# Performance work log

Hardware: AMD Instinct MI355X
Metric: run time of the kernel (lower is better)

Reference implementation:

```python
import jax, jax.numpy as jnp
import numpy as np

TEMP = 1.0  # composition softmax temperature

def _bank_topk(x, U, V, logits, top_k):
    # softmax over primitive logits, select top-k, renormalize, fused low-rank projection
    w = jax.nn.softmax(logits / TEMP)                     # [P]
    tw, ti = jax.lax.top_k(w, top_k)                      # [k], [k]
    tw = tw / tw.sum()
    Us = U[ti]                                            # [k, d_in, r]
    Vs = V[ti]                                            # [k, r, d_out]
    h = jnp.einsum('bsd,kdr->bksr', x, Us)                # low-rank bottleneck
    return jnp.einsum('bksr,kro,k->bso', h, Vs, tw)       # weighted fuse

def reference(x, q_U, q_V, k_U, k_V, v_U, v_V, q_logits, k_logits, v_logits, out_w, top_k):
    B, S, _ = x.shape
    H, D = 16, 64
    q = _bank_topk(x, q_U, q_V, q_logits, top_k)
    k = _bank_topk(x, k_U, k_V, k_logits, top_k)
    v = _bank_topk(x, v_U, v_V, v_logits, top_k)
    q = q.reshape(B, S, H, D).transpose(0, 2, 1, 3)       # [B,H,S,D]
    k = k.reshape(B, S, H, D).transpose(0, 2, 1, 3)
    v = v.reshape(B, S, H, D).transpose(0, 2, 1, 3)
    scale = 1.0 / jnp.sqrt(jnp.asarray(D, dtype=x.dtype))
    scores = jnp.einsum('bhqd,bhkd->bhqk', q, k) * scale  # [B,H,S,S]
    causal = jnp.triu(jnp.ones((S, S), dtype=bool), 1)
    scores = jnp.where(causal[None, None], jnp.finfo(x.dtype).min, scores)
    probs = jax.nn.softmax(scores, axis=-1)
    out = jnp.einsum('bhqk,bhkd->bhqd', probs, v)
    out = out.transpose(0, 2, 1, 3).reshape(B, S, H * D)
    return out @ out_w.T                                   # nn.Linear(H*D, d_model, bias=False)

def setup_inputs() -> dict:
    key = jax.random.key(0)
    ks = jax.random.split(key, 11)
    P, d, r = 16, 1024, 64
    B, S = 4, 1024
    f = jnp.float32
    inp = {
        'x': jax.random.normal(ks[0], (B, S, d), f),
        'q_U': jax.random.normal(ks[1], (P, d, r), f) * (1.0 / np.sqrt(d)),
        'q_V': jax.random.normal(ks[2], (P, r, d), f) * (1.0 / np.sqrt(r)),
        'k_U': jax.random.normal(ks[3], (P, d, r), f) * (1.0 / np.sqrt(d)),
        'k_V': jax.random.normal(ks[4], (P, r, d), f) * (1.0 / np.sqrt(r)),
        'v_U': jax.random.normal(ks[5], (P, d, r), f) * (1.0 / np.sqrt(d)),
        'v_V': jax.random.normal(ks[6], (P, r, d), f) * (1.0 / np.sqrt(r)),
        'q_logits': jax.random.normal(ks[7], (P,), f) * 0.01,
        'k_logits': jax.random.normal(ks[8], (P,), f) * 0.01,
        'v_logits': jax.random.normal(ks[9], (P,), f) * 0.01,
        'out_w': jax.random.normal(ks[10], (d, d), f) * (1.0 / np.sqrt(d)),
        'top_k': 4,
    }
    return inp
```

## Files before the change

### kernel.cpp

```cpp
#include <hip/hip_runtime.h>
#include <math.h>

#define D_MODEL 1024
#define RANK    64
#define PMAX    16
#define S_LEN   1024
#define HD      64
#define MROWS   4096
#define NHEAD   16
#define BATCH   4
#define KCMAX   (PMAX * RANK)

typedef short short8v __attribute__((ext_vector_type(8)));
typedef float floatx4 __attribute__((ext_vector_type(4)));

typedef __attribute__((address_space(1))) const unsigned int* gptr_t;
typedef __attribute__((address_space(3))) unsigned int* lptr_t;

static __device__ __forceinline__ void async16(const void* g, void* l) {
    __builtin_amdgcn_global_load_lds((gptr_t)g, (lptr_t)l, 16, 0, 0);
}

static __device__ __forceinline__ short f2bf(float f) {
    unsigned int u = __float_as_uint(f);
    u = (u + 0x7fffu + ((u >> 16) & 1u)) >> 16;
    return (short)u;
}

__global__ void topk_weights_kernel(const float* __restrict__ ql,
                                    const float* __restrict__ kl,
                                    const float* __restrict__ vl,
                                    const int* __restrict__ topk,
                                    int* __restrict__ idx_out,
                                    float* __restrict__ w_out) {
    int bank = threadIdx.x;
    if (bank >= 3) return;
    const float* lg = (bank == 0) ? ql : (bank == 1) ? kl : vl;
    int K = *topk; if (K < 1) K = 1; if (K > PMAX) K = PMAX;
    float l[PMAX];
    for (int i = 0; i < PMAX; ++i) l[i] = lg[i];
    bool used[PMAX];
    for (int i = 0; i < PMAX; ++i) used[i] = false;
    int   sel_i[PMAX];
    float sel_l[PMAX];
    for (int j = 0; j < K; ++j) {
        int best = -1; float bv = -INFINITY;
        for (int i = 0; i < PMAX; ++i)
            if (!used[i] && l[i] > bv) { bv = l[i]; best = i; }
        used[best] = true; sel_i[j] = best; sel_l[j] = bv;
    }
    float mx = sel_l[0];
    float e[PMAX];
    float sum = 0.f;
    for (int j = 0; j < K; ++j) { e[j] = __expf(sel_l[j] - mx); sum += e[j]; }
    float inv = 1.f / sum;
    for (int j = 0; j < PMAX; ++j) {
        idx_out[bank * PMAX + j] = (j < K) ? sel_i[j] : 0;
        w_out[bank * PMAX + j]   = (j < K) ? e[j] * inv : 0.f;
    }
}

__global__ __launch_bounds__(256) void convert_bf16_kernel(
    const float* __restrict__ src, short* __restrict__ dst, int n4) {
    int i = blockIdx.x * 256 + threadIdx.x;
    if (i < n4) {
        float4 f = ((const float4*)src)[i];
        short4 o;
        o.x = f2bf(f.x); o.y = f2bf(f.y); o.z = f2bf(f.z); o.w = f2bf(f.w);
        ((short4*)dst)[i] = o;
    }
}

__global__ __launch_bounds__(256) void prep_uv_kernel(
    const float* __restrict__ qU, const float* __restrict__ kU,
    const float* __restrict__ vU,
    const float* __restrict__ qV, const float* __restrict__ kV,
    const float* __restrict__ vV,
    const int* __restrict__ idx, const float* __restrict__ wsel,
    const int* __restrict__ topk,
    short* __restrict__ Uc, short* __restrict__ Vt) {
    int z    = blockIdx.z;
    int j    = blockIdx.y;
    int tile = blockIdx.x;
    int t    = threadIdx.x;
    int K = *topk; if (K < 1) K = 1; if (K > PMAX) K = PMAX;
    if (j >= K) return;
    __shared__ float T[64][65];
    int bank = (z < 3) ? z : z - 3;
    int p = idx[bank * PMAX + j];

    if (z < 3) {
        const float* U = (bank == 0) ? qU : (bank == 1) ? kU : vU;
        const float* src = U + (size_t)p * D_MODEL * RANK;
        short* dst = Uc + (size_t)bank * D_MODEL * KCMAX;
        int r4 = (t & 15) * 4;
        int dl = t >> 4;
#pragma unroll
        for (int i = 0; i < 4; ++i) {
            int d = tile * 64 + i * 16 + dl;
            float4 f = *(const float4*)&src[(size_t)d * RANK + r4];
            short4 o;
            o.x = f2bf(f.x); o.y = f2bf(f.y); o.z = f2bf(f.z); o.w = f2bf(f.w);
            *(short4*)&dst[(size_t)d * KCMAX + j * 64 + r4] = o;
        }
    } else {
        const float* V = (bank == 0) ? qV : (bank == 1) ? kV : vV;
        float wj = wsel[bank * PMAX + j];
        const float* src = V + (size_t)p * RANK * D_MODEL;
        int n0 = tile * 64;
        int nl = t & 63, rq = t >> 6;
#pragma unroll
        for (int i = 0; i < 16; ++i) {
            int rl = i * 4 + rq;
            T[nl][rl] = src[(size_t)rl * D_MODEL + n0 + nl] * wj;
        }
        __syncthreads();
        short* dst = Vt + (size_t)bank * D_MODEL * KCMAX;
        int rr = t >> 2;
#pragma unroll
        for (int i = 0; i < 4; ++i) {
            int c = (t & 3) * 16 + i * 4;
            short4 o;
            o.x = f2bf(T[rr][c + 0]); o.y = f2bf(T[rr][c + 1]);
            o.z = f2bf(T[rr][c + 2]); o.w = f2bf(T[rr][c + 3]);
            *(short4*)&dst[(size_t)(n0 + rr) * KCMAX + j * 64 + c] = o;
        }
    }
}

static __device__ __forceinline__ void mfma_gemm_tile(
    const short* __restrict__ A, const short* __restrict__ B, int kl,
    int lda, int ldb, int m0, int n0, short* As, short* Bs, floatx4 acc[4][4]) {
    const int t    = threadIdx.x;
    const int w    = t >> 6;
    const int lane = t & 63;
    const int wm   = w & 1, wn = w >> 1;
    const int colL = lane & 15, quad = lane >> 4;
    const int srow  = lane >> 2;
    const int skoff = (lane & 3) * 8;

#pragma unroll
    for (int i = 0; i < 4; ++i)
#pragma unroll
        for (int j = 0; j < 4; ++j) acc[i][j] = (floatx4){0.f, 0.f, 0.f, 0.f};

    for (int k0 = 0; k0 < kl; k0 += 32) {
        async16(A + (size_t)(m0 + w * 16 + srow) * lda + k0 + skoff,
                As + (w * 16 + srow) * 32 + skoff);
        async16(A + (size_t)(m0 + 64 + w * 16 + srow) * lda + k0 + skoff,
                As + (64 + w * 16 + srow) * 32 + skoff);
        async16(B + (size_t)(n0 + w * 16 + srow) * ldb + k0 + skoff,
                Bs + (w * 16 + srow) * 32 + skoff);
        async16(B + (size_t)(n0 + 64 + w * 16 + srow) * ldb + k0 + skoff,
                Bs + (64 + w * 16 + srow) * 32 + skoff);
        __syncthreads();
        short8v af[4], bf[4];
#pragma unroll
        for (int i = 0; i < 4; ++i)
            af[i] = *(const short8v*)&As[(wm * 64 + i * 16 + colL) * 32 + quad * 8];
#pragma unroll
        for (int j = 0; j < 4; ++j)
            bf[j] = *(const short8v*)&Bs[(wn * 64 + j * 16 + colL) * 32 + quad * 8];
#pragma unroll
        for (int i = 0; i < 4; ++i)
#pragma unroll
            for (int j = 0; j < 4; ++j)
                acc[i][j] = __builtin_amdgcn_mfma_f32_16x16x32_bf16(af[i], bf[j], acc[i][j], 0, 0, 0);
        __syncthreads();
    }
}

__global__ __launch_bounds__(256) void gemm_weff_kernel(
    const short* __restrict__ Vt, const short* __restrict__ Uc,
    const int* __restrict__ topk, short* __restrict__ Wt) {
    int K = *topk; if (K < 1) K = 1; if (K > PMAX) K = PMAX;
    int m0 = blockIdx.x * 128;
    int n0 = blockIdx.y * 128;
    int bank = blockIdx.z;
    __shared__ short As[128 * 32];
    __shared__ short Bs[128 * 32];
    floatx4 acc[4][4];
    mfma_gemm_tile(Vt + (size_t)bank * D_MODEL * KCMAX,
                   Uc + (size_t)bank * D_MODEL * KCMAX,
                   K * 64, KCMAX, KCMAX, m0, n0, As, Bs, acc);

    const int t = threadIdx.x, w = t >> 6, lane = t & 63;
    const int wm = w & 1, wn = w >> 1, colL = lane & 15, quad = lane >> 4;
    short* Wb = Wt + (size_t)bank * D_MODEL * D_MODEL;
#pragma unroll
    for (int i = 0; i < 4; ++i)
#pragma unroll
        for (int j = 0; j < 4; ++j)
#pragma unroll
            for (int r = 0; r < 4; ++r)
                Wb[(size_t)(m0 + wm * 64 + i * 16 + quad * 4 + r) * D_MODEL +
                   (n0 + wn * 64 + j * 16 + colL)] = f2bf(acc[i][j][r]);
}

__global__ __launch_bounds__(256) void gemm_qkv_kernel(
    const short* __restrict__ xb, const short* __restrict__ Wt,
    short* __restrict__ qkv) {
    int m0 = blockIdx.x * 128;
    int n0 = blockIdx.y * 128;
    int bank = blockIdx.z;
    __shared__ short As[128 * 32];
    __shared__ short Bs[128 * 32];
    floatx4 acc[4][4];
    mfma_gemm_tile(xb, Wt + (size_t)bank * D_MODEL * D_MODEL,
                   D_MODEL, D_MODEL, D_MODEL, m0, n0, As, Bs, acc);

    const int t = threadIdx.x, w = t >> 6, lane = t & 63;
    const int wm = w & 1, wn = w >> 1, colL = lane & 15, quad = lane >> 4;
    short* outp = qkv + (size_t)bank * MROWS * D_MODEL;
#pragma unroll
    for (int i = 0; i < 4; ++i)
#pragma unroll
        for (int j = 0; j < 4; ++j)
#pragma unroll
            for (int r = 0; r < 4; ++r) {
                int m = m0 + wm * 64 + i * 16 + quad * 4 + r;
                int n = n0 + wn * 64 + j * 16 + colL;
                int b = m >> 10, s = m & 1023;
                int head = n >> 6, d = n & 63;
                outp[(((size_t)(b * NHEAD + head) << 10) + s) * HD + d] = f2bf(acc[i][j][r]);
            }
}

__global__ __launch_bounds__(256) void gemm_proj_kernel(
    const short* __restrict__ attnb, const short* __restrict__ wb,
    float* __restrict__ outp) {
    int m0 = blockIdx.x * 128;
    int n0 = blockIdx.y * 128;
    __shared__ short As[128 * 32];
    __shared__ short Bs[128 * 32];
    floatx4 acc[4][4];
    mfma_gemm_tile(attnb, wb, D_MODEL, D_MODEL, D_MODEL, m0, n0, As, Bs, acc);

    const int t = threadIdx.x, w = t >> 6, lane = t & 63;
    const int wm = w & 1, wn = w >> 1, colL = lane & 15, quad = lane >> 4;
#pragma unroll
    for (int i = 0; i < 4; ++i)
#pragma unroll
        for (int j = 0; j < 4; ++j)
#pragma unroll
            for (int r = 0; r < 4; ++r)
                outp[(size_t)(m0 + wm * 64 + i * 16 + quad * 4 + r) * D_MODEL +
                     (n0 + wn * 64 + j * 16 + colL)] = acc[i][j][r];
}

__global__ __launch_bounds__(256) void attn_mfma_kernel(
    const short* __restrict__ qkv,
    short* __restrict__ attn_out) {
    const int t    = threadIdx.x;
    const int w    = t >> 6;
    const int lane = t & 63;
    const int col  = lane & 15;
    const int quad = lane >> 4;
    const int qt   = 15 - (int)blockIdx.x;
    const int bh   = blockIdx.y;
    const size_t HS   = (size_t)S_LEN * HD;
    const size_t BSTR = (size_t)MROWS * D_MODEL;
    const short* Qg = qkv + (size_t)bh * HS;
    const short* Kg = qkv + BSTR + (size_t)bh * HS;
    const short* Vg = qkv + 2 * BSTR + (size_t)bh * HS;

    __shared__ short Ks[64][72];
    __shared__ short Vt[64][72];
    __shared__ short Ps[4][16][72];

    const float SC = 0.125f * 1.44269504f;

    const int qrow = qt * 64 + w * 16 + col;
    short8v aq0 = *(const short8v*)(Qg + (size_t)qrow * HD + quad * 8);
    short8v aq1 = *(const short8v*)(Qg + (size_t)qrow * HD + 32 + quad * 8);
    floatx4 O0 = {0.f, 0.f, 0.f, 0.f}, O1 = O0, O2 = O0, O3 = O0;
    float mrow[4] = {-INFINITY, -INFINITY, -INFINITY, -INFINITY};
    float lrow[4] = {0.f, 0.f, 0.f, 0.f};

    for (int jt = 0; jt <= qt; ++jt) {
        __syncthreads();
        {
            int c = t;
            int key = c >> 3, db = (c & 7) * 8;
            *(short8v*)&Ks[key][db] =
                *(const short8v*)(Kg + (size_t)(jt * 64 + key) * HD + db);
            c = t + 256;
            key = c >> 3; db = (c & 7) * 8;
            *(short8v*)&Ks[key][db] =
                *(const short8v*)(Kg + (size_t)(jt * 64 + key) * HD + db);
        }
        {
            int k0 = (t & 31) * 2;
            int db = (t >> 5) * 8;
            short8v v0 = *(const short8v*)(Vg + (size_t)(jt * 64 + k0) * HD + db);
            short8v v1 = *(const short8v*)(Vg + (size_t)(jt * 64 + k0 + 1) * HD + db);
#pragma unroll
            for (int i = 0; i < 8; ++i) {
                unsigned int pk = (unsigned int)(unsigned short)v0[i] |
                                  ((unsigned int)(unsigned short)v1[i] << 16);
                *(unsigned int*)&Vt[db + i][k0] = pk;
            }
        }
        __syncthreads();

        const bool diag = (jt == qt);
        const int  nmax = diag ? w : 3;
        float sc[4][4];
#pragma unroll
        for (int n = 0; n < 4; ++n) {
            if (n <= nmax) {
                floatx4 c4 = {0.f, 0.f, 0.f, 0.f};
                short8v b0 = *(const short8v*)&Ks[n * 16 + col][quad * 8];
                short8v b1 = *(const short8v*)&Ks[n * 16 + col][32 + quad * 8];
                c4 = __builtin_amdgcn_mfma_f32_16x16x32_bf16(aq0, b0, c4, 0, 0, 0);
                c4 = __builtin_amdgcn_mfma_f32_16x16x32_bf16(aq1, b1, c4, 0, 0, 0);
#pragma unroll
                for (int r = 0; r < 4; ++r) {
                    float v = c4[r] * SC;
                    if (diag && n == w && col > quad * 4 + r) v = -INFINITY;
                    sc[n][r] = v;
                }
            } else {
#pragma unroll
                for (int r = 0; r < 4; ++r) sc[n][r] = -INFINITY;
            }
        }
        float pv[4][4];
#pragma unroll
        for (int r = 0; r < 4; ++r) {
            float tm = fmaxf(fmaxf(sc[0][r], sc[1][r]), fmaxf(sc[2][r], sc[3][r]));
            tm = fmaxf(tm, __shfl_xor(tm, 1));
            tm = fmaxf(tm, __shfl_xor(tm, 2));
            tm = fmaxf(tm, __shfl_xor(tm, 4));
            tm = fmaxf(tm, __shfl_xor(tm, 8));
            float mnew  = fmaxf(mrow[r], tm);
            float alpha = exp2f(mrow[r] - mnew);
            float ps = 0.f;
#pragma unroll
            for (int n = 0; n < 4; ++n) {
                float p = exp2f(sc[n][r] - mnew);
                pv[n][r] = p;
                ps += p;
            }
            ps += __shfl_xor(ps, 1);
            ps += __shfl_xor(ps, 2);
            ps += __shfl_xor(ps, 4);
            ps += __shfl_xor(ps, 8);
            lrow[r] = lrow[r] * alpha + ps;
            mrow[r] = mnew;
            O0[r] *= alpha; O1[r] *= alpha; O2[r] *= alpha; O3[r] *= alpha;
        }
#pragma unroll
        for (int n = 0; n < 4; ++n)
#pragma unroll
            for (int r = 0; r < 4; ++r)
                Ps[w][quad * 4 + r][n * 16 + col] = f2bf(pv[n][r]);
        const int ksmax = diag ? (w >> 1) : 1;
#pragma unroll
        for (int ks = 0; ks < 2; ++ks) {
            if (ks > ksmax) break;
            short8v ap  = *(const short8v*)&Ps[w][col][ks * 32 + quad * 8];
            short8v bv0 = *(const short8v*)&Vt[0  + col][ks * 32 + quad * 8];
            short8v bv1 = *(const short8v*)&Vt[16 + col][ks * 32 + quad * 8];
            short8v bv2 = *(const short8v*)&Vt[32 + col][ks * 32 + quad * 8];
            short8v bv3 = *(const short8v*)&Vt[48 + col][ks * 32 + quad * 8];
            O0 = __builtin_amdgcn_mfma_f32_16x16x32_bf16(ap, bv0, O0, 0, 0, 0);
            O1 = __builtin_amdgcn_mfma_f32_16x16x32_bf16(ap, bv1, O1, 0, 0, 0);
            O2 = __builtin_amdgcn_mfma_f32_16x16x32_bf16(ap, bv2, O2, 0, 0, 0);
            O3 = __builtin_amdgcn_mfma_f32_16x16x32_bf16(ap, bv3, O3, 0, 0, 0);
        }
    }
    const int b  = bh >> 4;
    const int hh = bh & 15;
    short* orow = attn_out +
        ((size_t)(b * S_LEN) + qt * 64 + w * 16) * D_MODEL + hh * 64;
#pragma unroll
    for (int r = 0; r < 4; ++r) {
        float inv = 1.f / lrow[r];
        short* prw = orow + (size_t)(quad * 4 + r) * D_MODEL;
        prw[0  + col] = f2bf(O0[r] * inv);
        prw[16 + col] = f2bf(O1[r] * inv);
        prw[32 + col] = f2bf(O2[r] * inv);
        prw[48 + col] = f2bf(O3[r] * inv);
    }
}

extern "C" void kernel_launch(void* const* d_in, const int* in_sizes, int n_in,
                              void* d_out, int out_size, void* d_ws, size_t ws_size,
                              hipStream_t stream) {
    const float* x    = (const float*)d_in[0];
    const float* qU   = (const float*)d_in[1];
    const float* qV   = (const float*)d_in[2];
    const float* kU   = (const float*)d_in[3];
    const float* kV   = (const float*)d_in[4];
    const float* vU   = (const float*)d_in[5];
    const float* vV   = (const float*)d_in[6];
    const float* qlg  = (const float*)d_in[7];
    const float* klg  = (const float*)d_in[8];
    const float* vlg  = (const float*)d_in[9];
    const float* outw = (const float*)d_in[10];
    const int*   topk = (const int*)d_in[11];
    float* outp = (float*)d_out;

    char* ws = (char*)d_ws;
    int*   idxp = (int*)ws;
    float* wp   = (float*)(ws + 256);
    short* xb   = (short*)(ws + 512);
    short* Uc   = xb + (size_t)MROWS * D_MODEL;
    short* Vt   = Uc + (size_t)3 * D_MODEL * KCMAX;
    short* wb   = Vt + (size_t)3 * D_MODEL * KCMAX;
    short* Wt   = wb + (size_t)D_MODEL * D_MODEL;
    short* qkvb = Wt + (size_t)3 * D_MODEL * D_MODEL;
    short* attnb = qkvb + (size_t)3 * MROWS * D_MODEL;

    topk_weights_kernel<<<1, 64, 0, stream>>>(qlg, klg, vlg, topk, idxp, wp);
    convert_bf16_kernel<<<(MROWS * D_MODEL / 4 + 255) / 256, 256, 0, stream>>>(
        x, xb, MROWS * D_MODEL / 4);
    convert_bf16_kernel<<<(D_MODEL * D_MODEL / 4 + 255) / 256, 256, 0, stream>>>(
        outw, wb, D_MODEL * D_MODEL / 4);
    prep_uv_kernel<<<dim3(16, 16, 6), 256, 0, stream>>>(
        qU, kU, vU, qV, kV, vV, idxp, wp, topk, Uc, Vt);
    gemm_weff_kernel<<<dim3(8, 8, 3), 256, 0, stream>>>(Vt, Uc, topk, Wt);
    gemm_qkv_kernel<<<dim3(32, 8, 3), 256, 0, stream>>>(xb, Wt, qkvb);
    attn_mfma_kernel<<<dim3(16, 64), 256, 0, stream>>>(qkvb, attnb);
    gemm_proj_kernel<<<dim3(32, 8), 256, 0, stream>>>(attnb, wb, outp);
}
```

Before: 243.3 us.

## Pair causal query tiles per block, widen KV tiles, swizzle block order for XCDs

```diff
diff --git a/kernel.cpp b/kernel.cpp
--- a/kernel.cpp
+++ b/kernel.cpp
@@ -174,9 +174,10 @@
     const short* __restrict__ Vt, const short* __restrict__ Uc,
     const int* __restrict__ topk, short* __restrict__ Wt) {
     int K = *topk; if (K < 1) K = 1; if (K > PMAX) K = PMAX;
-    int m0 = blockIdx.x * 128;
-    int n0 = blockIdx.y * 128;
-    int bank = blockIdx.z;
+    int id = blockIdx.x + 8 * (blockIdx.y + 8 * blockIdx.z);
+    int sw = (id & 7) * 24 + (id >> 3);
+    int m0 = (sw & 7) * 128; int rest = sw >> 3;
+    int n0 = (rest & 7) * 128; int bank = rest >> 3;
     __shared__ short As[128 * 32];
     __shared__ short Bs[128 * 32];
     floatx4 acc[4][4];
@@ -200,9 +201,10 @@
 __global__ __launch_bounds__(256) void gemm_qkv_kernel(
     const short* __restrict__ xb, const short* __restrict__ Wt,
     short* __restrict__ qkv) {
-    int m0 = blockIdx.x * 128;
-    int n0 = blockIdx.y * 128;
-    int bank = blockIdx.z;
+    int id = blockIdx.x + 32 * (blockIdx.y + 8 * blockIdx.z);
+    int sw = (id & 7) * 96 + (id >> 3);
+    int m0 = (sw & 31) * 128; int rest = sw >> 5;
+    int n0 = (rest & 7) * 128; int bank = rest >> 3;
     __shared__ short As[128 * 32];
     __shared__ short Bs[128 * 32];
     floatx4 acc[4][4];
@@ -229,8 +231,10 @@
 __global__ __launch_bounds__(256) void gemm_proj_kernel(
     const short* __restrict__ attnb, const short* __restrict__ wb,
     float* __restrict__ outp) {
-    int m0 = blockIdx.x * 128;
-    int n0 = blockIdx.y * 128;
+    int id = blockIdx.x + 32 * blockIdx.y;
+    int sw = (id & 7) * 32 + (id >> 3);
+    int m0 = (sw & 31) * 128;
+    int n0 = (sw >> 5) * 128;
     __shared__ short As[128 * 32];
     __shared__ short Bs[128 * 32];
     floatx4 acc[4][4];
@@ -256,132 +260,138 @@
     const int lane = t & 63;
     const int col  = lane & 15;
     const int quad = lane >> 4;
-    const int qt   = 15 - (int)blockIdx.x;
-    const int bh   = blockIdx.y;
+    int id = blockIdx.x + 8 * blockIdx.y;
+    int sw = (id & 7) * 64 + (id >> 3);
+    const int pr = sw & 7;
+    const int bh = sw >> 3;
     const size_t HS   = (size_t)S_LEN * HD;
     const size_t BSTR = (size_t)MROWS * D_MODEL;
     const short* Qg = qkv + (size_t)bh * HS;
     const short* Kg = qkv + BSTR + (size_t)bh * HS;
     const short* Vg = qkv + 2 * BSTR + (size_t)bh * HS;
 
-    __shared__ short Ks[64][72];
-    __shared__ short Vt[64][72];
-    __shared__ short Ps[4][16][72];
+    __shared__ short Ks[128][72];
+    __shared__ short Vt[64][136];
+    __shared__ short Ps[4][16][136];
 
     const float SC = 0.125f * 1.44269504f;
 
-    const int qrow = qt * 64 + w * 16 + col;
-    short8v aq0 = *(const short8v*)(Qg + (size_t)qrow * HD + quad * 8);
-    short8v aq1 = *(const short8v*)(Qg + (size_t)qrow * HD + 32 + quad * 8);
-    floatx4 O0 = {0.f, 0.f, 0.f, 0.f}, O1 = O0, O2 = O0, O3 = O0;
-    float mrow[4] = {-INFINITY, -INFINITY, -INFINITY, -INFINITY};
-    float lrow[4] = {0.f, 0.f, 0.f, 0.f};
-
-    for (int jt = 0; jt <= qt; ++jt) {
-        __syncthreads();
-        {
-            int c = t;
-            int key = c >> 3, db = (c & 7) * 8;
-            *(short8v*)&Ks[key][db] =
-                *(const short8v*)(Kg + (size_t)(jt * 64 + key) * HD + db);
-            c = t + 256;
-            key = c >> 3; db = (c & 7) * 8;
-            *(short8v*)&Ks[key][db] =
-                *(const short8v*)(Kg + (size_t)(jt * 64 + key) * HD + db);
+    for (int ph = 0; ph < 2; ++ph) {
+        const int qt = ph ? (15 - pr) : pr;
+        const int qb = qt * 4 + w;
+        const int qrow = qt * 64 + w * 16 + col;
+        short8v aq0 = *(const short8v*)(Qg + (size_t)qrow * HD + quad * 8);
+        short8v aq1 = *(const short8v*)(Qg + (size_t)qrow * HD + 32 + quad * 8);
+        floatx4 O0 = {0.f, 0.f, 0.f, 0.f}, O1 = O0, O2 = O0, O3 = O0;
+        float mrow[4] = {-INFINITY, -INFINITY, -INFINITY, -INFINITY};
+        float lrow[4] = {0.f, 0.f, 0.f, 0.f};
+        const int nkv = (qt + 2) >> 1;
+
+        for (int jt = 0; jt < nkv; ++jt) {
+            __syncthreads();
+#pragma unroll
+            for (int it = 0; it < 4; ++it) {
+                int idx = t + it * 256;
+                int key = idx >> 3, db = (idx & 7) * 8;
+                *(short8v*)&Ks[key][db] =
+                    *(const short8v*)(Kg + (size_t)(jt * 128 + key) * HD + db);
+            }
+#pragma unroll
+            for (int it = 0; it < 2; ++it) {
+                int idx = t + it * 256;
+                int k0 = (idx & 63) * 2;
+                int db = (idx >> 6) * 8;
+                short8v v0 = *(const short8v*)(Vg + (size_t)(jt * 128 + k0) * HD + db);
+                short8v v1 = *(const short8v*)(Vg + (size_t)(jt * 128 + k0 + 1) * HD + db);
+#pragma unroll
+                for (int i = 0; i < 8; ++i) {
+                    unsigned int pk = (unsigned int)(unsigned short)v0[i] |
+                                      ((unsigned int)(unsigned short)v1[i] << 16);
+                    *(unsigned int*)&Vt[db + i][k0] = pk;
+                }
+            }
+            __syncthreads();
+
+            float sc[8][4];
+            const int base = jt * 8;
+#pragma unroll
+            for (int n = 0; n < 8; ++n) {
+                int rel = qb - (base + n);
+                if (rel >= 0) {
+                    floatx4 c4 = {0.f, 0.f, 0.f, 0.f};
+                    short8v b0 = *(const short8v*)&Ks[n * 16 + col][quad * 8];
+                    short8v b1 = *(const short8v*)&Ks[n * 16 + col][32 + quad * 8];
+                    c4 = __builtin_amdgcn_mfma_f32_16x16x32_bf16(aq0, b0, c4, 0, 0, 0);
+                    c4 = __builtin_amdgcn_mfma_f32_16x16x32_bf16(aq1, b1, c4, 0, 0, 0);
+#pragma unroll
+                    for (int r = 0; r < 4; ++r) {
+                        float v = c4[r] * SC;
+                        if (rel == 0 && col > quad * 4 + r) v = -INFINITY;
+                        sc[n][r] = v;
+                    }
+                } else {
+#pragma unroll
+                    for (int r = 0; r < 4; ++r) sc[n][r] = -INFINITY;
+                }
+            }
+#pragma unroll
+            for (int r = 0; r < 4; ++r) {
+                float tm = sc[0][r];
+#pragma unroll
+                for (int n = 1; n < 8; ++n) tm = fmaxf(tm, sc[n][r]);
+                tm = fmaxf(tm, __shfl_xor(tm, 1));
+                tm = fmaxf(tm, __shfl_xor(tm, 2));
+                tm = fmaxf(tm, __shfl_xor(tm, 4));
+                tm = fmaxf(tm, __shfl_xor(tm, 8));
+                if (__any(tm > mrow[r] + 8.0f)) {
+                    float mnew  = fmaxf(mrow[r], tm);
+                    float alpha = exp2f(mrow[r] - mnew);
+                    lrow[r] *= alpha;
+                    O0[r] *= alpha; O1[r] *= alpha; O2[r] *= alpha; O3[r] *= alpha;
+                    mrow[r] = mnew;
+                }
+                float ps = 0.f;
+#pragma unroll
+                for (int n = 0; n < 8; ++n) {
+                    float p = exp2f(sc[n][r] - mrow[r]);
+                    ps += p;
+                    Ps[w][quad * 4 + r][n * 16 + col] = f2bf(p);
+                }
+                ps += __shfl_xor(ps, 1);
+                ps += __shfl_xor(ps, 2);
+                ps += __shfl_xor(ps, 4);
+                ps += __shfl_xor(ps, 8);
+                lrow[r] += ps;
+            }
+            int lim = qb * 16 + 15 - (jt << 7);
+            int ksm = lim >> 5; if (ksm > 3) ksm = 3;
+#pragma unroll
+            for (int ks = 0; ks < 4; ++ks) {
+                if (ks > ksm) break;
+                short8v ap  = *(const short8v*)&Ps[w][col][ks * 32 + quad * 8];
+                short8v bv0 = *(const short8v*)&Vt[0  + col][ks * 32 + quad * 8];
+                short8v bv1 = *(const short8v*)&Vt[16 + col][ks * 32 + quad * 8];
+                short8v bv2 = *(const short8v*)&Vt[32 + col][ks * 32 + quad * 8];
+                short8v bv3 = *(const short8v*)&Vt[48 + col][ks * 32 + quad * 8];
+                O0 = __builtin_amdgcn_mfma_f32_16x16x32_bf16(ap, bv0, O0, 0, 0, 0);
+                O1 = __builtin_amdgcn_mfma_f32_16x16x32_bf16(ap, bv1, O1, 0, 0, 0);
+                O2 = __builtin_amdgcn_mfma_f32_16x16x32_bf16(ap, bv2, O2, 0, 0, 0);
+                O3 = __builtin_amdgcn_mfma_f32_16x16x32_bf16(ap, bv3, O3, 0, 0, 0);
+            }
         }
-        {
-            int k0 = (t & 31) * 2;
-            int db = (t >> 5) * 8;
-            short8v v0 = *(const short8v*)(Vg + (size_t)(jt * 64 + k0) * HD + db);
-            short8v v1 = *(const short8v*)(Vg + (size_t)(jt * 64 + k0 + 1) * HD + db);
-#pragma unroll
-            for (int i = 0; i < 8; ++i) {
-                unsigned int pk = (unsigned int)(unsigned short)v0[i] |
-                                  ((unsigned int)(unsigned short)v1[i] << 16);
-                *(unsigned int*)&Vt[db + i][k0] = pk;
-            }
+        const int b  = bh >> 4;
+        const int hh = bh & 15;
+        short* orow = attn_out +
+            ((size_t)(b * S_LEN) + qt * 64 + w * 16) * D_MODEL + hh * 64;
+#pragma unroll
+        for (int r = 0; r < 4; ++r) {
+            float inv = 1.f / lrow[r];
+            short* prw = orow + (size_t)(quad * 4 + r) * D_MODEL;
+            prw[0  + col] = f2bf(O0[r] * inv);
+            prw[16 + col] = f2bf(O1[r] * inv);
+            prw[32 + col] = f2bf(O2[r] * inv);
+            prw[48 + col] = f2bf(O3[r] * inv);
         }
-        __syncthreads();
-
-        const bool diag = (jt == qt);
-        const int  nmax = diag ? w : 3;
-        float sc[4][4];
-#pragma unroll
-        for (int n = 0; n < 4; ++n) {
-            if (n <= nmax) {
-                floatx4 c4 = {0.f, 0.f, 0.f, 0.f};
-                short8v b0 = *(const short8v*)&Ks[n * 16 + col][quad * 8];
-                short8v b1 = *(const short8v*)&Ks[n * 16 + col][32 + quad * 8];
-                c4 = __builtin_amdgcn_mfma_f32_16x16x32_bf16(aq0, b0, c4, 0, 0, 0);
-                c4 = __builtin_amdgcn_mfma_f32_16x16x32_bf16(aq1, b1, c4, 0, 0, 0);
-#pragma unroll
-                for (int r = 0; r < 4; ++r) {
-                    float v = c4[r] * SC;
-                    if (diag && n == w && col > quad * 4 + r) v = -INFINITY;
-                    sc[n][r] = v;
-                }
-            } else {
-#pragma unroll
-                for (int r = 0; r < 4; ++r) sc[n][r] = -INFINITY;
-            }
-        }
-        float pv[4][4];
-#pragma unroll
-        for (int r = 0; r < 4; ++r) {
-            float tm = fmaxf(fmaxf(sc[0][r], sc[1][r]), fmaxf(sc[2][r], sc[3][r]));
-            tm = fmaxf(tm, __shfl_xor(tm, 1));
-            tm = fmaxf(tm, __shfl_xor(tm, 2));
-            tm = fmaxf(tm, __shfl_xor(tm, 4));
-            tm = fmaxf(tm, __shfl_xor(tm, 8));
-            float mnew  = fmaxf(mrow[r], tm);
-            float alpha = exp2f(mrow[r] - mnew);
-            float ps = 0.f;
-#pragma unroll
-            for (int n = 0; n < 4; ++n) {
-                float p = exp2f(sc[n][r] - mnew);
-                pv[n][r] = p;
-                ps += p;
-            }
-            ps += __shfl_xor(ps, 1);
-            ps += __shfl_xor(ps, 2);
-            ps += __shfl_xor(ps, 4);
-            ps += __shfl_xor(ps, 8);
-            lrow[r] = lrow[r] * alpha + ps;
-            mrow[r] = mnew;
-            O0[r] *= alpha; O1[r] *= alpha; O2[r] *= alpha; O3[r] *= alpha;
-        }
-#pragma unroll
-        for (int n = 0; n < 4; ++n)
-#pragma unroll
-            for (int r = 0; r < 4; ++r)
-                Ps[w][quad * 4 + r][n * 16 + col] = f2bf(pv[n][r]);
-        const int ksmax = diag ? (w >> 1) : 1;
-#pragma unroll
-        for (int ks = 0; ks < 2; ++ks) {
-            if (ks > ksmax) break;
-            short8v ap  = *(const short8v*)&Ps[w][col][ks * 32 + quad * 8];
-            short8v bv0 = *(const short8v*)&Vt[0  + col][ks * 32 + quad * 8];
-            short8v bv1 = *(const short8v*)&Vt[16 + col][ks * 32 + quad * 8];
-            short8v bv2 = *(const short8v*)&Vt[32 + col][ks * 32 + quad * 8];
-            short8v bv3 = *(const short8v*)&Vt[48 + col][ks * 32 + quad * 8];
-            O0 = __builtin_amdgcn_mfma_f32_16x16x32_bf16(ap, bv0, O0, 0, 0, 0);
-            O1 = __builtin_amdgcn_mfma_f32_16x16x32_bf16(ap, bv1, O1, 0, 0, 0);
-            O2 = __builtin_amdgcn_mfma_f32_16x16x32_bf16(ap, bv2, O2, 0, 0, 0);
-            O3 = __builtin_amdgcn_mfma_f32_16x16x32_bf16(ap, bv3, O3, 0, 0, 0);
-        }
-    }
-    const int b  = bh >> 4;
-    const int hh = bh & 15;
-    short* orow = attn_out +
-        ((size_t)(b * S_LEN) + qt * 64 + w * 16) * D_MODEL + hh * 64;
-#pragma unroll
-    for (int r = 0; r < 4; ++r) {
-        float inv = 1.f / lrow[r];
-        short* prw = orow + (size_t)(quad * 4 + r) * D_MODEL;
-        prw[0  + col] = f2bf(O0[r] * inv);
-        prw[16 + col] = f2bf(O1[r] * inv);
-        prw[32 + col] = f2bf(O2[r] * inv);
-        prw[48 + col] = f2bf(O3[r] * inv);
     }
 }
 
@@ -422,6 +432,6 @@
         qU, kU, vU, qV, kV, vV, idxp, wp, topk, Uc, Vt);
     gemm_weff_kernel<<<dim3(8, 8, 3), 256, 0, stream>>>(Vt, Uc, topk, Wt);
     gemm_qkv_kernel<<<dim3(32, 8, 3), 256, 0, stream>>>(xb, Wt, qkvb);
-    attn_mfma_kernel<<<dim3(16, 64), 256, 0, stream>>>(qkvb, attnb);
+    attn_mfma_kernel<<<dim3(8, 64), 256, 0, stream>>>(qkvb, attnb);
     gemm_proj_kernel<<<dim3(32, 8), 256, 0, stream>>>(attnb, wb, outp);
 }
```

Measured after the change: 222.8 us. -8.4%, faster.
